# Performance work log

Hardware: AMD Instinct MI355X
Metric: run time of the kernel (lower is better)

Reference implementation:

```python
import jax, jax.numpy as jnp
import numpy as np

N_NODES = 10000
N_EDGES = 640000
N_GRAPHS = 64
D = 128
N_BLOCKS = 2
NEG_SLOPE = 0.01  # F.leaky_relu default


def setup_inputs() -> dict:
    key = jax.random.key(0)
    ks = jax.random.split(key, 9)
    x = jax.random.normal(ks[0], (N_NODES, D), dtype=jnp.float32)
    edge_src = jax.random.randint(ks[1], (N_EDGES,), 0, N_NODES, dtype=jnp.int32)
    edge_dst = jax.random.randint(ks[2], (N_EDGES,), 0, N_NODES, dtype=jnp.int32)
    graph_ids = jnp.sort(jax.random.randint(ks[3], (N_NODES,), 0, N_GRAPHS, dtype=jnp.int32))
    s = 1.414 / np.sqrt(D)  # xavier-normal-ish scale
    Wfc = jax.random.normal(ks[4], (N_BLOCKS, D, D), dtype=jnp.float32) * s
    bfc = jnp.zeros((N_BLOCKS, D), dtype=jnp.float32)
    wl = jax.random.normal(ks[5], (N_BLOCKS, D), dtype=jnp.float32) * s
    wr = jax.random.normal(ks[6], (N_BLOCKS, D), dtype=jnp.float32) * s
    Wres = jax.random.normal(ks[7], (N_BLOCKS, D, D), dtype=jnp.float32) * s
    return {"x": x, "edge_src": edge_src, "edge_dst": edge_dst, "graph_ids": graph_ids,
            "Wfc": Wfc, "bfc": bfc, "wl": wl, "wr": wr, "Wres": Wres}


def _gat_block(x, edge_src, edge_dst, Wfc_b, bfc_b, wl_b, wr_b, Wres_b):
    # node projections: nn.Linear -> x @ W^T + b
    feat = x @ Wfc_b.T + bfc_b                       # [N, D]
    a_self = feat @ wl_b                              # [N] self_a (dst side)
    a_nb = feat @ wr_b                                # [N] attn  (src side)
    # per-edge score: leaky_relu(self_a[dst] + attn[src])
    s = a_self[edge_dst] + a_nb[edge_src]             # [E]
    s = jnp.where(s >= 0, s, NEG_SLOPE * s)
    # segment softmax over incoming edges of each dst node
    m = jax.ops.segment_max(s, edge_dst, num_segments=N_NODES)   # [N]
    e = jnp.exp(s - m[edge_dst])                                  # [E]
    denom = jax.ops.segment_sum(e, edge_dst, num_segments=N_NODES)
    w = e / denom[edge_dst]                                       # [E]
    # attention-weighted neighbor aggregation
    accum = jax.ops.segment_sum(w[:, None] * feat[edge_src], edge_dst,
                                num_segments=N_NODES)             # [N, D]
    # residual (in_size == out_size -> res_fc, no bias), then relu
    out = accum + x @ Wres_b.T
    return jax.nn.relu(out)


def reference(x, edge_src, edge_dst, graph_ids, Wfc, bfc, wl, wr, Wres):
    blocks = [
        _gat_block(x, edge_src, edge_dst, Wfc[b], bfc[b], wl[b], wr[b], Wres[b])
        for b in range(N_BLOCKS)
    ]
    h = jnp.concatenate(blocks, axis=1)               # mode='concat' -> [N, 2*D]
    # dgl.sum_nodes: per-graph sum pooling
    phis = jax.ops.segment_sum(h, graph_ids, num_segments=N_GRAPHS)  # [G, 2*D]
    return h, phis
```

## Files before the change

kernel.cpp:

```cpp
#include <hip/hip_runtime.h>
#include <hip/hip_bf16.h>
#include <math.h>

#define N_NODES 10000
#define N_EDGES 640000
#define N_GRAPHS 64
#define DIM 128
#define NEG_SLOPE 0.01f
#define NB_CSR 128
#define EDGES_PER_BLK (N_EDGES / NB_CSR)

typedef __attribute__((ext_vector_type(8))) short bf16x8;
typedef __attribute__((ext_vector_type(4))) float f32x4;


__device__ __forceinline__ unsigned short f2bf(float f) {
    __hip_bfloat16 h = __float2bfloat16(f);
    return *reinterpret_cast<unsigned short*>(&h);
}

__global__ __launch_bounds__(1024) void csr_hist(const int4* __restrict__ edst4,
                                                 int* __restrict__ bh) {
    __shared__ int hist[N_NODES];
    const int blk = blockIdx.x;
    const int t = threadIdx.x;
    for (int n = t; n < N_NODES; n += 1024) hist[n] = 0;
    __syncthreads();
    const int base4 = blk * (EDGES_PER_BLK / 4);
    for (int i = t; i < EDGES_PER_BLK / 4; i += 1024) {
        int4 d = edst4[base4 + i];
        atomicAdd(&hist[d.x], 1);
        atomicAdd(&hist[d.y], 1);
        atomicAdd(&hist[d.z], 1);
        atomicAdd(&hist[d.w], 1);
    }
    __syncthreads();
    int* dst = bh + (size_t)blk * N_NODES;
    for (int n = t; n < N_NODES; n += 1024) dst[n] = hist[n];
}

__global__ __launch_bounds__(256) void csr_node_scan(int* __restrict__ bh,
                                                     int* __restrict__ deg) {
    int n4 = blockIdx.x * 256 + threadIdx.x;
    if (n4 >= N_NODES / 4) return;
    int4 run = {0, 0, 0, 0};
    for (int blk = 0; blk < NB_CSR; ++blk) {
        int4* p = reinterpret_cast<int4*>(bh + (size_t)blk * N_NODES) + n4;
        int4 v = *p;
        *p = run;
        run.x += v.x; run.y += v.y; run.z += v.z; run.w += v.w;
    }
    reinterpret_cast<int4*>(deg)[n4] = run;
}

__global__ __launch_bounds__(1024) void scan_deg(const int* __restrict__ deg,
                                                 int* __restrict__ rowptr,
                                                 float* __restrict__ phis) {
    __shared__ int sdata[1024];
    const int tid = threadIdx.x;
    for (int i = tid; i < N_GRAPHS * 2 * DIM; i += 1024) phis[i] = 0.f;

    const int base = tid * 10;
    int cnt = N_NODES - base;
    if (cnt < 0) cnt = 0;
    if (cnt > 10) cnt = 10;
    int local[10];
    int s = 0;
    for (int i = 0; i < cnt; ++i) { local[i] = s; s += deg[base + i]; }
    sdata[tid] = s;
    __syncthreads();
    for (int off = 1; off < 1024; off <<= 1) {
        int v = 0;
        if (tid >= off) v = sdata[tid - off];
        __syncthreads();
        if (tid >= off) sdata[tid] += v;
        __syncthreads();
    }
    int pre = (tid == 0) ? 0 : sdata[tid - 1];
    for (int i = 0; i < cnt; ++i) rowptr[base + i] = pre + local[i];
    if (tid == 1023) rowptr[N_NODES] = sdata[1023];
}

__global__ __launch_bounds__(1024) void csr_scatter(
    const int4* __restrict__ esrc4, const int4* __restrict__ edst4,
    const int* __restrict__ rowptr, const int* __restrict__ bh,
    int* __restrict__ csr_src) {
    __shared__ int cur[N_NODES];
    const int blk = blockIdx.x;
    const int t = threadIdx.x;
    const int* boff = bh + (size_t)blk * N_NODES;
    for (int n = t; n < N_NODES; n += 1024) cur[n] = rowptr[n] + boff[n];
    __syncthreads();
    const int base4 = blk * (EDGES_PER_BLK / 4);
    for (int i = t; i < EDGES_PER_BLK / 4; i += 1024) {
        int4 s = esrc4[base4 + i];
        int4 d = edst4[base4 + i];
        csr_src[atomicAdd(&cur[d.x], 1)] = s.x;
        csr_src[atomicAdd(&cur[d.y], 1)] = s.y;
        csr_src[atomicAdd(&cur[d.z], 1)] = s.z;
        csr_src[atomicAdd(&cur[d.w], 1)] = s.w;
    }
}

__global__ __launch_bounds__(256) void gemm_mfma(
    const float* __restrict__ x, const float* __restrict__ Wfc,
    const float* __restrict__ bfc, const float* __restrict__ Wres,
    const float* __restrict__ wl, const float* __restrict__ wr,
    float* __restrict__ resid, unsigned short* __restrict__ feat_b16,
    float* __restrict__ a_self, float* __restrict__ a_nb) {
    const int which = blockIdx.y & 1;
    const int b = blockIdx.y >> 1;
    const float* __restrict__ W = (which ? Wres : Wfc) + b * DIM * DIM;
    const int n0 = blockIdx.x * 64;
    const int t = threadIdx.x;

    __shared__ unsigned short xs[64][136];
    __shared__ unsigned short wsh[128][136];

    {
        const int r = t >> 2, qq = t & 3;
        const int n = n0 + r;
        ushort4* drow = reinterpret_cast<ushort4*>(&xs[r][qq * 32]);
        if (n < N_NODES) {
            const float4* p = reinterpret_cast<const float4*>(x + (size_t)n * DIM + qq * 32);
#pragma unroll
            for (int i = 0; i < 8; ++i) {
                float4 v = p[i];
                ushort4 u;
                u.x = f2bf(v.x); u.y = f2bf(v.y); u.z = f2bf(v.z); u.w = f2bf(v.w);
                drow[i] = u;
            }
        } else {
            ushort4 z = {0, 0, 0, 0};
#pragma unroll
            for (int i = 0; i < 8; ++i) drow[i] = z;
        }
    }
    {
        const int rw = t >> 1, hh = t & 1;
        const float4* p = reinterpret_cast<const float4*>(W + (size_t)rw * DIM + hh * 64);
        ushort4* drow = reinterpret_cast<ushort4*>(&wsh[rw][hh * 64]);
#pragma unroll
        for (int i = 0; i < 16; ++i) {
            float4 v = p[i];
            ushort4 u;
            u.x = f2bf(v.x); u.y = f2bf(v.y); u.z = f2bf(v.z); u.w = f2bf(v.w);
            drow[i] = u;
        }
    }
    __syncthreads();

    const int wave = t >> 6, lane = t & 63;
    const int quad = lane >> 4, jc = lane & 15;
    const int m0 = wave * 16;

    bf16x8 af[4];
#pragma unroll
    for (int ks = 0; ks < 4; ++ks)
        af[ks] = *reinterpret_cast<const bf16x8*>(&xs[m0 + jc][ks * 32 + quad * 8]);

    f32x4 accs[8];
    float ps[4] = {0.f, 0.f, 0.f, 0.f}, pr[4] = {0.f, 0.f, 0.f, 0.f};
#pragma unroll
    for (int jt = 0; jt < 8; ++jt) {
        f32x4 acc = {0.f, 0.f, 0.f, 0.f};
#pragma unroll
        for (int ks = 0; ks < 4; ++ks) {
            bf16x8 bfr = *reinterpret_cast<const bf16x8*>(
                &wsh[jt * 16 + jc][ks * 32 + quad * 8]);
            acc = __builtin_amdgcn_mfma_f32_16x16x32_bf16(af[ks], bfr, acc, 0, 0, 0);
        }
        if (!which) {
            float bias = bfc[b * DIM + jt * 16 + jc];
            acc[0] += bias; acc[1] += bias; acc[2] += bias; acc[3] += bias;
            float wlv = wl[b * DIM + jt * 16 + jc];
            float wrv = wr[b * DIM + jt * 16 + jc];
#pragma unroll
            for (int r2 = 0; r2 < 4; ++r2) { ps[r2] += acc[r2] * wlv; pr[r2] += acc[r2] * wrv; }
        }
        accs[jt] = acc;
    }

    __syncthreads();

    if (!which) {
#pragma unroll
        for (int off = 8; off > 0; off >>= 1) {
#pragma unroll
            for (int r2 = 0; r2 < 4; ++r2) {
                ps[r2] += __shfl_xor(ps[r2], off, 64);
                pr[r2] += __shfl_xor(pr[r2], off, 64);
            }
        }
        if (jc == 0) {
#pragma unroll
            for (int r2 = 0; r2 < 4; ++r2) {
                int n = n0 + m0 + quad * 4 + r2;
                if (n < N_NODES) {
                    a_self[b * N_NODES + n] = ps[r2];
                    a_nb[b * N_NODES + n] = pr[r2];
                }
            }
        }
#pragma unroll
        for (int jt = 0; jt < 8; ++jt)
#pragma unroll
            for (int r2 = 0; r2 < 4; ++r2)
                xs[m0 + quad * 4 + r2][jt * 16 + jc] = f2bf(accs[jt][r2]);
        __syncthreads();
        const int r = t >> 2, qq = t & 3;
        const int n = n0 + r;
        if (n < N_NODES) {
            uint4* dst = reinterpret_cast<uint4*>(
                feat_b16 + ((size_t)b * N_NODES + n) * DIM + qq * 32);
            const uint4* srcp = reinterpret_cast<const uint4*>(&xs[r][qq * 32]);
#pragma unroll
            for (int i = 0; i < 4; ++i) dst[i] = srcp[i];
        }
    } else {
        float* fs = reinterpret_cast<float*>(wsh);
#pragma unroll
        for (int jt = 0; jt < 8; ++jt)
#pragma unroll
            for (int r2 = 0; r2 < 4; ++r2)
                fs[(m0 + quad * 4 + r2) * 136 + jt * 16 + jc] = accs[jt][r2];
        __syncthreads();
        const int r = t >> 2, qq = t & 3;
        const int n = n0 + r;
        if (n < N_NODES) {
            float4* dst = reinterpret_cast<float4*>(
                resid + ((size_t)b * N_NODES + n) * DIM + qq * 32);
            const float4* srcp = reinterpret_cast<const float4*>(&fs[r * 136 + qq * 32]);
#pragma unroll
            for (int i = 0; i < 8; ++i) dst[i] = srcp[i];
        }
    }
}

__global__ __launch_bounds__(256) void aggregate(
    const unsigned short* __restrict__ feat_b16, const float* __restrict__ resid,
    const float* __restrict__ a_self, const float* __restrict__ a_nb,
    const int* __restrict__ rowptr, const int* __restrict__ csr_src,
    float* __restrict__ out) {
    const int wave = threadIdx.x >> 6;
    const int lane = threadIdx.x & 63;
    const int n = blockIdx.x * 4 + wave;
    const int b = blockIdx.y;
    const int q = lane >> 4;
    const int l16 = lane & 15;
    const int start = rowptr[n];
    const int end = rowptr[n + 1];

    const float* __restrict__ anb = a_nb + b * N_NODES;
    const uint4* __restrict__ fb =
        reinterpret_cast<const uint4*>(feat_b16 + (size_t)b * N_NODES * DIM);
    const float asl = a_self[b * N_NODES + n];

    float acc[8];
#pragma unroll
    for (int k = 0; k < 8; ++k) acc[k] = 0.f;
    float dpart = 0.f;

    for (int c = start; c < end; c += 64) {
        int j = c + lane;
        float e = 0.f;
        int src = 0;
        if (j < end) {
            src = csr_src[j];
            float s = asl + anb[src];
            s = (s >= 0.f) ? s : NEG_SLOPE * s;
            e = __expf(s);
        }
        dpart += e;
        int cnt = end - c;
        if (cnt > 64) cnt = 64;
        int iters = (cnt + 3) >> 2;

        float w0 = __shfl(e, q, 64);
        int s0 = __shfl(src, q, 64);
        uint4 f0 = fb[(size_t)s0 * 16 + l16];

        for (int i2 = 0; i2 < iters - 1; ++i2) {
            int idx = (i2 + 1) * 4 + q;
            float w1 = __shfl(e, idx, 64);
            int s1 = __shfl(src, idx, 64);
            uint4 f1 = fb[(size_t)s1 * 16 + l16];
#pragma unroll
            for (int k = 0; k < 4; ++k) {
                unsigned int u = (&f0.x)[k];
                float lo = __uint_as_float(u << 16);
                float hi = __uint_as_float(u & 0xffff0000u);
                acc[2 * k]     += w0 * lo;
                acc[2 * k + 1] += w0 * hi;
            }
            w0 = w1; f0 = f1;
        }
#pragma unroll
        for (int k = 0; k < 4; ++k) {
            unsigned int u = (&f0.x)[k];
            float lo = __uint_as_float(u << 16);
            float hi = __uint_as_float(u & 0xffff0000u);
            acc[2 * k]     += w0 * lo;
            acc[2 * k + 1] += w0 * hi;
        }
    }

#pragma unroll
    for (int k = 0; k < 8; ++k) {
        acc[k] += __shfl_xor(acc[k], 16, 64);
        acc[k] += __shfl_xor(acc[k], 32, 64);
    }
    float denom = dpart;
#pragma unroll
    for (int off = 32; off > 0; off >>= 1) denom += __shfl_xor(denom, off, 64);

    if (q == 0) {
        float inv = (end > start) ? 1.f / denom : 0.f;
        const float4* rr = reinterpret_cast<const float4*>(
            resid + ((size_t)b * N_NODES + n) * DIM);
        float4 r0 = rr[l16 * 2];
        float4 r1 = rr[l16 * 2 + 1];
        float4 o0, o1;
        o0.x = fmaxf(acc[0] * inv + r0.x, 0.f);
        o0.y = fmaxf(acc[1] * inv + r0.y, 0.f);
        o0.z = fmaxf(acc[2] * inv + r0.z, 0.f);
        o0.w = fmaxf(acc[3] * inv + r0.w, 0.f);
        o1.x = fmaxf(acc[4] * inv + r1.x, 0.f);
        o1.y = fmaxf(acc[5] * inv + r1.y, 0.f);
        o1.z = fmaxf(acc[6] * inv + r1.z, 0.f);
        o1.w = fmaxf(acc[7] * inv + r1.w, 0.f);
        float4* po = reinterpret_cast<float4*>(out + (size_t)n * (2 * DIM) + b * DIM);
        po[l16 * 2] = o0;
        po[l16 * 2 + 1] = o1;
    }
}

__device__ int lower_bound_dev(const int* __restrict__ a, int n, int key) {
    int lo = 0, hi = n;
    while (lo < hi) {
        int mid = (lo + hi) >> 1;
        if (a[mid] < key) lo = mid + 1;
        else hi = mid;
    }
    return lo;
}

__global__ __launch_bounds__(256) void pool_graphs(
    const float* __restrict__ h, const int* __restrict__ gids,
    float* __restrict__ phis) {
    const int g = blockIdx.x;
    const int chunk = blockIdx.y;
    const int tid = threadIdx.x;
    int lo = lower_bound_dev(gids, N_NODES, g);
    int hi = lower_bound_dev(gids, N_NODES, g + 1);
    float acc = 0.f;
    for (int n = lo + chunk; n < hi; n += 16) acc += h[(size_t)n * (2 * DIM) + tid];
    if (acc != 0.f) atomicAdd(&phis[(size_t)g * (2 * DIM) + tid], acc);
}

extern "C" void kernel_launch(void* const* d_in, const int* in_sizes, int n_in,
                              void* d_out, int out_size, void* d_ws, size_t ws_size,
                              hipStream_t stream) {
    const float* x    = (const float*)d_in[0];
    const int* esrc   = (const int*)d_in[1];
    const int* edst   = (const int*)d_in[2];
    const int* gids   = (const int*)d_in[3];
    const float* Wfc  = (const float*)d_in[4];
    const float* bfc  = (const float*)d_in[5];
    const float* wl   = (const float*)d_in[6];
    const float* wr   = (const float*)d_in[7];
    const float* Wres = (const float*)d_in[8];
    float* out = (float*)d_out;

    char* ws = (char*)d_ws;
    float* resid   = (float*)(ws + 0);
    float* a_self  = (float*)(ws + 10240000);
    float* a_nb    = (float*)(ws + 10320000);
    int*   deg     = (int*)(ws + 10400000);
    int*   rowptr  = (int*)(ws + 10440000);
    int*   csr_src = (int*)(ws + 10480032);
    unsigned short* feat_b16 = (unsigned short*)(ws + 13040032);
    int*   bh      = (int*)(ws + 18160032);

    float* phis = out + (size_t)N_NODES * 2 * DIM;

    csr_hist<<<NB_CSR, 1024, 0, stream>>>((const int4*)edst, bh);
    csr_node_scan<<<(N_NODES / 4 + 255) / 256, 256, 0, stream>>>(bh, deg);
    scan_deg<<<1, 1024, 0, stream>>>(deg, rowptr, phis);
    csr_scatter<<<NB_CSR, 1024, 0, stream>>>(
        (const int4*)esrc, (const int4*)edst, rowptr, bh, csr_src);

    gemm_mfma<<<dim3((N_NODES + 63) / 64, 4), 256, 0, stream>>>(
        x, Wfc, bfc, Wres, wl, wr, resid, feat_b16, a_self, a_nb);
    aggregate<<<dim3(2500, 2), 256, 0, stream>>>(
        feat_b16, resid, a_self, a_nb, rowptr, csr_src, out);
    pool_graphs<<<dim3(N_GRAPHS, 16), 256, 0, stream>>>(out, gids, phis);
}
```

Measured before the change: 169.8 us.

## Fuse histogram with projection GEMM and split each node's edges across two waves

The CSR histogram blocks and the MFMA projection GEMM blocks now run in one launch, with blocks picking their role by index, so the independent GEMM overlaps the histogram and one kernel launch is removed. The histogram blocks drop from 1024 to 256 threads to match the GEMM's block size. Aggregation now gives each destination node two waves that take alternating 64-edge chunks. Their partial sums and denominators are combined through shared memory before the epilogue. This doubles parallelism for the memory-bound gather, at the cost of an extra block sync and shared-memory reduction.

```diff
diff --git a/kernel.cpp b/kernel.cpp
--- a/kernel.cpp
+++ b/kernel.cpp
@@ -9,6 +9,8 @@
 #define NEG_SLOPE 0.01f
 #define NB_CSR 128
 #define EDGES_PER_BLK (N_EDGES / NB_CSR)
+#define G_TILES 157
+#define G_BLOCKS (G_TILES * 4)
 
 typedef __attribute__((ext_vector_type(8))) short bf16x8;
 typedef __attribute__((ext_vector_type(4))) float f32x4;
@@ -19,24 +21,164 @@
     return *reinterpret_cast<unsigned short*>(&h);
 }
 
-__global__ __launch_bounds__(1024) void csr_hist(const int4* __restrict__ edst4,
-                                                 int* __restrict__ bh) {
-    __shared__ int hist[N_NODES];
-    const int blk = blockIdx.x;
+__global__ __launch_bounds__(256) void gemm_hist(
+    const int4* __restrict__ edst4, int* __restrict__ bh,
+    const float* __restrict__ x, const float* __restrict__ Wfc,
+    const float* __restrict__ bfc, const float* __restrict__ Wres,
+    const float* __restrict__ wl, const float* __restrict__ wr,
+    float* __restrict__ resid, unsigned short* __restrict__ feat_b16,
+    float* __restrict__ a_self, float* __restrict__ a_nb) {
+    __shared__ char smem[52224];
     const int t = threadIdx.x;
-    for (int n = t; n < N_NODES; n += 1024) hist[n] = 0;
+
+    if (blockIdx.x < NB_CSR) {
+        int* hist = reinterpret_cast<int*>(smem);
+        const int blk = blockIdx.x;
+        for (int n = t; n < N_NODES; n += 256) hist[n] = 0;
+        __syncthreads();
+        const int base4 = blk * (EDGES_PER_BLK / 4);
+        for (int i = t; i < EDGES_PER_BLK / 4; i += 256) {
+            int4 d = edst4[base4 + i];
+            atomicAdd(&hist[d.x], 1);
+            atomicAdd(&hist[d.y], 1);
+            atomicAdd(&hist[d.z], 1);
+            atomicAdd(&hist[d.w], 1);
+        }
+        __syncthreads();
+        int* dst = bh + (size_t)blk * N_NODES;
+        for (int n = t; n < N_NODES; n += 256) dst[n] = hist[n];
+        return;
+    }
+
+    const int blk = blockIdx.x - NB_CSR;
+    const int which = blk & 1;
+    const int b = (blk >> 1) & 1;
+    const int n0 = (blk >> 2) * 64;
+    const float* __restrict__ W = (which ? Wres : Wfc) + b * DIM * DIM;
+
+    typedef unsigned short us_row[136];
+    us_row* xs = reinterpret_cast<us_row*>(smem);
+    us_row* wsh = reinterpret_cast<us_row*>(smem + 17408);
+
+    {
+        const int r = t >> 2, qq = t & 3;
+        const int n = n0 + r;
+        ushort4* drow = reinterpret_cast<ushort4*>(&xs[r][qq * 32]);
+        if (n < N_NODES) {
+            const float4* p = reinterpret_cast<const float4*>(x + (size_t)n * DIM + qq * 32);
+#pragma unroll
+            for (int i = 0; i < 8; ++i) {
+                float4 v = p[i];
+                ushort4 u;
+                u.x = f2bf(v.x); u.y = f2bf(v.y); u.z = f2bf(v.z); u.w = f2bf(v.w);
+                drow[i] = u;
+            }
+        } else {
+            ushort4 z = {0, 0, 0, 0};
+#pragma unroll
+            for (int i = 0; i < 8; ++i) drow[i] = z;
+        }
+    }
+    {
+        const int rw = t >> 1, hh = t & 1;
+        const float4* p = reinterpret_cast<const float4*>(W + (size_t)rw * DIM + hh * 64);
+        ushort4* drow = reinterpret_cast<ushort4*>(&wsh[rw][hh * 64]);
+#pragma unroll
+        for (int i = 0; i < 16; ++i) {
+            float4 v = p[i];
+            ushort4 u;
+            u.x = f2bf(v.x); u.y = f2bf(v.y); u.z = f2bf(v.z); u.w = f2bf(v.w);
+            drow[i] = u;
+        }
+    }
     __syncthreads();
-    const int base4 = blk * (EDGES_PER_BLK / 4);
-    for (int i = t; i < EDGES_PER_BLK / 4; i += 1024) {
-        int4 d = edst4[base4 + i];
-        atomicAdd(&hist[d.x], 1);
-        atomicAdd(&hist[d.y], 1);
-        atomicAdd(&hist[d.z], 1);
-        atomicAdd(&hist[d.w], 1);
-    }
+
+    const int wave = t >> 6, lane = t & 63;
+    const int quad = lane >> 4, jc = lane & 15;
+    const int m0 = wave * 16;
+
+    bf16x8 af[4];
+#pragma unroll
+    for (int ks = 0; ks < 4; ++ks)
+        af[ks] = *reinterpret_cast<const bf16x8*>(&xs[m0 + jc][ks * 32 + quad * 8]);
+
+    f32x4 accs[8];
+    float ps[4] = {0.f, 0.f, 0.f, 0.f}, pr[4] = {0.f, 0.f, 0.f, 0.f};
+#pragma unroll
+    for (int jt = 0; jt < 8; ++jt) {
+        f32x4 acc = {0.f, 0.f, 0.f, 0.f};
+#pragma unroll
+        for (int ks = 0; ks < 4; ++ks) {
+            bf16x8 bfr = *reinterpret_cast<const bf16x8*>(
+                &wsh[jt * 16 + jc][ks * 32 + quad * 8]);
+            acc = __builtin_amdgcn_mfma_f32_16x16x32_bf16(af[ks], bfr, acc, 0, 0, 0);
+        }
+        if (!which) {
+            float bias = bfc[b * DIM + jt * 16 + jc];
+            acc[0] += bias; acc[1] += bias; acc[2] += bias; acc[3] += bias;
+            float wlv = wl[b * DIM + jt * 16 + jc];
+            float wrv = wr[b * DIM + jt * 16 + jc];
+#pragma unroll
+            for (int r2 = 0; r2 < 4; ++r2) { ps[r2] += acc[r2] * wlv; pr[r2] += acc[r2] * wrv; }
+        }
+        accs[jt] = acc;
+    }
+
     __syncthreads();
-    int* dst = bh + (size_t)blk * N_NODES;
-    for (int n = t; n < N_NODES; n += 1024) dst[n] = hist[n];
+
+    if (!which) {
+#pragma unroll
+        for (int off = 8; off > 0; off >>= 1) {
+#pragma unroll
+            for (int r2 = 0; r2 < 4; ++r2) {
+                ps[r2] += __shfl_xor(ps[r2], off, 64);
+                pr[r2] += __shfl_xor(pr[r2], off, 64);
+            }
+        }
+        if (jc == 0) {
+#pragma unroll
+            for (int r2 = 0; r2 < 4; ++r2) {
+                int n = n0 + m0 + quad * 4 + r2;
+                if (n < N_NODES) {
+                    a_self[b * N_NODES + n] = ps[r2];
+                    a_nb[b * N_NODES + n] = pr[r2];
+                }
+            }
+        }
+#pragma unroll
+        for (int jt = 0; jt < 8; ++jt)
+#pragma unroll
+            for (int r2 = 0; r2 < 4; ++r2)
+                xs[m0 + quad * 4 + r2][jt * 16 + jc] = f2bf(accs[jt][r2]);
+        __syncthreads();
+        const int r = t >> 2, qq = t & 3;
+        const int n = n0 + r;
+        if (n < N_NODES) {
+            uint4* dst = reinterpret_cast<uint4*>(
+                feat_b16 + ((size_t)b * N_NODES + n) * DIM + qq * 32);
+            const uint4* srcp = reinterpret_cast<const uint4*>(&xs[r][qq * 32]);
+#pragma unroll
+            for (int i = 0; i < 4; ++i) dst[i] = srcp[i];
+        }
+    } else {
+        float* fs = reinterpret_cast<float*>(smem);
+        __syncthreads();
+#pragma unroll
+        for (int jt = 0; jt < 8; ++jt)
+#pragma unroll
+            for (int r2 = 0; r2 < 4; ++r2)
+                fs[(m0 + quad * 4 + r2) * 136 + jt * 16 + jc] = accs[jt][r2];
+        __syncthreads();
+        const int r = t >> 2, qq = t & 3;
+        const int n = n0 + r;
+        if (n < N_NODES) {
+            float4* dst = reinterpret_cast<float4*>(
+                resid + ((size_t)b * N_NODES + n) * DIM + qq * 32);
+            const float4* srcp = reinterpret_cast<const float4*>(&fs[r * 136 + qq * 32]);
+#pragma unroll
+            for (int i = 0; i < 8; ++i) dst[i] = srcp[i];
+        }
+    }
 }
 
 __global__ __launch_bounds__(256) void csr_node_scan(int* __restrict__ bh,
@@ -102,155 +244,25 @@
     }
 }
 
-__global__ __launch_bounds__(256) void gemm_mfma(
-    const float* __restrict__ x, const float* __restrict__ Wfc,
-    const float* __restrict__ bfc, const float* __restrict__ Wres,
-    const float* __restrict__ wl, const float* __restrict__ wr,
-    float* __restrict__ resid, unsigned short* __restrict__ feat_b16,
-    float* __restrict__ a_self, float* __restrict__ a_nb) {
-    const int which = blockIdx.y & 1;
-    const int b = blockIdx.y >> 1;
-    const float* __restrict__ W = (which ? Wres : Wfc) + b * DIM * DIM;
-    const int n0 = blockIdx.x * 64;
-    const int t = threadIdx.x;
-
-    __shared__ unsigned short xs[64][136];
-    __shared__ unsigned short wsh[128][136];
-
-    {
-        const int r = t >> 2, qq = t & 3;
-        const int n = n0 + r;
-        ushort4* drow = reinterpret_cast<ushort4*>(&xs[r][qq * 32]);
-        if (n < N_NODES) {
-            const float4* p = reinterpret_cast<const float4*>(x + (size_t)n * DIM + qq * 32);
-#pragma unroll
-            for (int i = 0; i < 8; ++i) {
-                float4 v = p[i];
-                ushort4 u;
-                u.x = f2bf(v.x); u.y = f2bf(v.y); u.z = f2bf(v.z); u.w = f2bf(v.w);
-                drow[i] = u;
-            }
-        } else {
-            ushort4 z = {0, 0, 0, 0};
-#pragma unroll
-            for (int i = 0; i < 8; ++i) drow[i] = z;
-        }
-    }
-    {
-        const int rw = t >> 1, hh = t & 1;
-        const float4* p = reinterpret_cast<const float4*>(W + (size_t)rw * DIM + hh * 64);
-        ushort4* drow = reinterpret_cast<ushort4*>(&wsh[rw][hh * 64]);
-#pragma unroll
-        for (int i = 0; i < 16; ++i) {
-            float4 v = p[i];
-            ushort4 u;
-            u.x = f2bf(v.x); u.y = f2bf(v.y); u.z = f2bf(v.z); u.w = f2bf(v.w);
-            drow[i] = u;
-        }
-    }
-    __syncthreads();
-
-    const int wave = t >> 6, lane = t & 63;
-    const int quad = lane >> 4, jc = lane & 15;
-    const int m0 = wave * 16;
-
-    bf16x8 af[4];
-#pragma unroll
-    for (int ks = 0; ks < 4; ++ks)
-        af[ks] = *reinterpret_cast<const bf16x8*>(&xs[m0 + jc][ks * 32 + quad * 8]);
-
-    f32x4 accs[8];
-    float ps[4] = {0.f, 0.f, 0.f, 0.f}, pr[4] = {0.f, 0.f, 0.f, 0.f};
-#pragma unroll
-    for (int jt = 0; jt < 8; ++jt) {
-        f32x4 acc = {0.f, 0.f, 0.f, 0.f};
-#pragma unroll
-        for (int ks = 0; ks < 4; ++ks) {
-            bf16x8 bfr = *reinterpret_cast<const bf16x8*>(
-                &wsh[jt * 16 + jc][ks * 32 + quad * 8]);
-            acc = __builtin_amdgcn_mfma_f32_16x16x32_bf16(af[ks], bfr, acc, 0, 0, 0);
-        }
-        if (!which) {
-            float bias = bfc[b * DIM + jt * 16 + jc];
-            acc[0] += bias; acc[1] += bias; acc[2] += bias; acc[3] += bias;
-            float wlv = wl[b * DIM + jt * 16 + jc];
-            float wrv = wr[b * DIM + jt * 16 + jc];
-#pragma unroll
-            for (int r2 = 0; r2 < 4; ++r2) { ps[r2] += acc[r2] * wlv; pr[r2] += acc[r2] * wrv; }
-        }
-        accs[jt] = acc;
-    }
-
-    __syncthreads();
-
-    if (!which) {
-#pragma unroll
-        for (int off = 8; off > 0; off >>= 1) {
-#pragma unroll
-            for (int r2 = 0; r2 < 4; ++r2) {
-                ps[r2] += __shfl_xor(ps[r2], off, 64);
-                pr[r2] += __shfl_xor(pr[r2], off, 64);
-            }
-        }
-        if (jc == 0) {
-#pragma unroll
-            for (int r2 = 0; r2 < 4; ++r2) {
-                int n = n0 + m0 + quad * 4 + r2;
-                if (n < N_NODES) {
-                    a_self[b * N_NODES + n] = ps[r2];
-                    a_nb[b * N_NODES + n] = pr[r2];
-                }
-            }
-        }
-#pragma unroll
-        for (int jt = 0; jt < 8; ++jt)
-#pragma unroll
-            for (int r2 = 0; r2 < 4; ++r2)
-                xs[m0 + quad * 4 + r2][jt * 16 + jc] = f2bf(accs[jt][r2]);
-        __syncthreads();
-        const int r = t >> 2, qq = t & 3;
-        const int n = n0 + r;
-        if (n < N_NODES) {
-            uint4* dst = reinterpret_cast<uint4*>(
-                feat_b16 + ((size_t)b * N_NODES + n) * DIM + qq * 32);
-            const uint4* srcp = reinterpret_cast<const uint4*>(&xs[r][qq * 32]);
-#pragma unroll
-            for (int i = 0; i < 4; ++i) dst[i] = srcp[i];
-        }
-    } else {
-        float* fs = reinterpret_cast<float*>(wsh);
-#pragma unroll
-        for (int jt = 0; jt < 8; ++jt)
-#pragma unroll
-            for (int r2 = 0; r2 < 4; ++r2)
-                fs[(m0 + quad * 4 + r2) * 136 + jt * 16 + jc] = accs[jt][r2];
-        __syncthreads();
-        const int r = t >> 2, qq = t & 3;
-        const int n = n0 + r;
-        if (n < N_NODES) {
-            float4* dst = reinterpret_cast<float4*>(
-                resid + ((size_t)b * N_NODES + n) * DIM + qq * 32);
-            const float4* srcp = reinterpret_cast<const float4*>(&fs[r * 136 + qq * 32]);
-#pragma unroll
-            for (int i = 0; i < 8; ++i) dst[i] = srcp[i];
-        }
-    }
-}
-
 __global__ __launch_bounds__(256) void aggregate(
     const unsigned short* __restrict__ feat_b16, const float* __restrict__ resid,
     const float* __restrict__ a_self, const float* __restrict__ a_nb,
     const int* __restrict__ rowptr, const int* __restrict__ csr_src,
     float* __restrict__ out) {
-    const int wave = threadIdx.x >> 6;
-    const int lane = threadIdx.x & 63;
-    const int n = blockIdx.x * 4 + wave;
+    const int t = threadIdx.x;
+    const int wave = t >> 6, lane = t & 63;
+    const int nl = wave >> 1;
+    const int sub = wave & 1;
+    const int n = blockIdx.x * 2 + nl;
     const int b = blockIdx.y;
     const int q = lane >> 4;
     const int l16 = lane & 15;
     const int start = rowptr[n];
     const int end = rowptr[n + 1];
 
+    __shared__ float pacc[2][2][128];
+    __shared__ float pden[2][2];
+
     const float* __restrict__ anb = a_nb + b * N_NODES;
     const uint4* __restrict__ fb =
         reinterpret_cast<const uint4*>(feat_b16 + (size_t)b * N_NODES * DIM);
@@ -261,7 +273,7 @@
     for (int k = 0; k < 8; ++k) acc[k] = 0.f;
     float dpart = 0.f;
 
-    for (int c = start; c < end; c += 64) {
+    for (int c = start + sub * 64; c < end; c += 128) {
         int j = c + lane;
         float e = 0.f;
         int src = 0;
@@ -310,28 +322,29 @@
         acc[k] += __shfl_xor(acc[k], 16, 64);
         acc[k] += __shfl_xor(acc[k], 32, 64);
     }
-    float denom = dpart;
-#pragma unroll
-    for (int off = 32; off > 0; off >>= 1) denom += __shfl_xor(denom, off, 64);
+    float den = dpart;
+#pragma unroll
+    for (int off = 32; off > 0; off >>= 1) den += __shfl_xor(den, off, 64);
 
     if (q == 0) {
+#pragma unroll
+        for (int k = 0; k < 8; ++k) pacc[nl][sub][l16 * 8 + k] = acc[k];
+    }
+    if (lane == 0) pden[nl][sub] = den;
+    __syncthreads();
+
+    if (sub == 0) {
+        float denom = pden[nl][0] + pden[nl][1];
         float inv = (end > start) ? 1.f / denom : 0.f;
-        const float4* rr = reinterpret_cast<const float4*>(
-            resid + ((size_t)b * N_NODES + n) * DIM);
-        float4 r0 = rr[l16 * 2];
-        float4 r1 = rr[l16 * 2 + 1];
-        float4 o0, o1;
-        o0.x = fmaxf(acc[0] * inv + r0.x, 0.f);
-        o0.y = fmaxf(acc[1] * inv + r0.y, 0.f);
-        o0.z = fmaxf(acc[2] * inv + r0.z, 0.f);
-        o0.w = fmaxf(acc[3] * inv + r0.w, 0.f);
-        o1.x = fmaxf(acc[4] * inv + r1.x, 0.f);
-        o1.y = fmaxf(acc[5] * inv + r1.y, 0.f);
-        o1.z = fmaxf(acc[6] * inv + r1.z, 0.f);
-        o1.w = fmaxf(acc[7] * inv + r1.w, 0.f);
-        float4* po = reinterpret_cast<float4*>(out + (size_t)n * (2 * DIM) + b * DIM);
-        po[l16 * 2] = o0;
-        po[l16 * 2 + 1] = o1;
+        int c0 = lane * 2;
+        float a0 = pacc[nl][0][c0] + pacc[nl][1][c0];
+        float a1 = pacc[nl][0][c0 + 1] + pacc[nl][1][c0 + 1];
+        float2 r = reinterpret_cast<const float2*>(
+            resid + ((size_t)b * N_NODES + n) * DIM)[lane];
+        float2 o;
+        o.x = fmaxf(a0 * inv + r.x, 0.f);
+        o.y = fmaxf(a1 * inv + r.y, 0.f);
+        reinterpret_cast<float2*>(out + (size_t)n * (2 * DIM) + b * DIM)[lane] = o;
     }
 }
 
@@ -384,15 +397,15 @@
 
     float* phis = out + (size_t)N_NODES * 2 * DIM;
 
-    csr_hist<<<NB_CSR, 1024, 0, stream>>>((const int4*)edst, bh);
+    gemm_hist<<<NB_CSR + G_BLOCKS, 256, 0, stream>>>(
+        (const int4*)edst, bh, x, Wfc, bfc, Wres, wl, wr,
+        resid, feat_b16, a_self, a_nb);
     csr_node_scan<<<(N_NODES / 4 + 255) / 256, 256, 0, stream>>>(bh, deg);
     scan_deg<<<1, 1024, 0, stream>>>(deg, rowptr, phis);
     csr_scatter<<<NB_CSR, 1024, 0, stream>>>(
         (const int4*)esrc, (const int4*)edst, rowptr, bh, csr_src);
 
-    gemm_mfma<<<dim3((N_NODES + 63) / 64, 4), 256, 0, stream>>>(
-        x, Wfc, bfc, Wres, wl, wr, resid, feat_b16, a_self, a_nb);
-    aggregate<<<dim3(2500, 2), 256, 0, stream>>>(
+    aggregate<<<dim3(5000, 2), 256, 0, stream>>>(
         feat_b16, resid, a_self, a_nb, rowptr, csr_src, out);
     pool_graphs<<<dim3(N_GRAPHS, 16), 256, 0, stream>>>(out, gids, phis);
 }
```

Result: no change. 172.4 us (+1.6%).

## Fuse edge score computation into CSR scatter, shrink residual and histogram to 16-bit

Applied to the files above, without the earlier changes.

Moves the GEMM ahead of CSR construction so csr_scatter can compute the leaky-relu exp score per edge for both blocks and store (src, exp) pairs. The aggregate kernel then reads precomputed weights instead of gathering a_nb per edge. The residual is stored as bf16 instead of fp32, and per-block histograms as 16-bit, which roughly halves those buffers' traffic. The costs are more scatter work and random reads inside csr_scatter, twice the CSR storage, and lower residual precision. Skipping the max subtraction in the softmax risks overflow.

```diff
diff --git a/kernel.cpp b/kernel.cpp
--- a/kernel.cpp
+++ b/kernel.cpp
@@ -19,8 +19,130 @@
     return *reinterpret_cast<unsigned short*>(&h);
 }
 
+__global__ __launch_bounds__(256) void gemm_mfma(
+    const float* __restrict__ x, const float* __restrict__ Wfc,
+    const float* __restrict__ bfc, const float* __restrict__ Wres,
+    const float* __restrict__ wl, const float* __restrict__ wr,
+    unsigned short* __restrict__ resid_b16, unsigned short* __restrict__ feat_b16,
+    float* __restrict__ a_self, float* __restrict__ a_nb) {
+    const int which = blockIdx.y & 1;
+    const int b = blockIdx.y >> 1;
+    const float* __restrict__ W = (which ? Wres : Wfc) + b * DIM * DIM;
+    const int n0 = blockIdx.x * 64;
+    const int t = threadIdx.x;
+
+    __shared__ unsigned short xs[64][136];
+    __shared__ unsigned short wsh[128][136];
+
+    {
+        const int r = t >> 2, qq = t & 3;
+        const int n = n0 + r;
+        ushort4* drow = reinterpret_cast<ushort4*>(&xs[r][qq * 32]);
+        if (n < N_NODES) {
+            const float4* p = reinterpret_cast<const float4*>(x + (size_t)n * DIM + qq * 32);
+#pragma unroll
+            for (int i = 0; i < 8; ++i) {
+                float4 v = p[i];
+                ushort4 u;
+                u.x = f2bf(v.x); u.y = f2bf(v.y); u.z = f2bf(v.z); u.w = f2bf(v.w);
+                drow[i] = u;
+            }
+        } else {
+            ushort4 z = {0, 0, 0, 0};
+#pragma unroll
+            for (int i = 0; i < 8; ++i) drow[i] = z;
+        }
+    }
+    {
+        const int rw = t >> 1, hh = t & 1;
+        const float4* p = reinterpret_cast<const float4*>(W + (size_t)rw * DIM + hh * 64);
+        ushort4* drow = reinterpret_cast<ushort4*>(&wsh[rw][hh * 64]);
+#pragma unroll
+        for (int i = 0; i < 16; ++i) {
+            float4 v = p[i];
+            ushort4 u;
+            u.x = f2bf(v.x); u.y = f2bf(v.y); u.z = f2bf(v.z); u.w = f2bf(v.w);
+            drow[i] = u;
+        }
+    }
+    __syncthreads();
+
+    const int wave = t >> 6, lane = t & 63;
+    const int quad = lane >> 4, jc = lane & 15;
+    const int m0 = wave * 16;
+
+    bf16x8 af[4];
+#pragma unroll
+    for (int ks = 0; ks < 4; ++ks)
+        af[ks] = *reinterpret_cast<const bf16x8*>(&xs[m0 + jc][ks * 32 + quad * 8]);
+
+    f32x4 accs[8];
+    float ps[4] = {0.f, 0.f, 0.f, 0.f}, pr[4] = {0.f, 0.f, 0.f, 0.f};
+#pragma unroll
+    for (int jt = 0; jt < 8; ++jt) {
+        f32x4 acc = {0.f, 0.f, 0.f, 0.f};
+#pragma unroll
+        for (int ks = 0; ks < 4; ++ks) {
+            bf16x8 bfr = *reinterpret_cast<const bf16x8*>(
+                &wsh[jt * 16 + jc][ks * 32 + quad * 8]);
+            acc = __builtin_amdgcn_mfma_f32_16x16x32_bf16(af[ks], bfr, acc, 0, 0, 0);
+        }
+        if (!which) {
+            float bias = bfc[b * DIM + jt * 16 + jc];
+            acc[0] += bias; acc[1] += bias; acc[2] += bias; acc[3] += bias;
+            float wlv = wl[b * DIM + jt * 16 + jc];
+            float wrv = wr[b * DIM + jt * 16 + jc];
+#pragma unroll
+            for (int r2 = 0; r2 < 4; ++r2) { ps[r2] += acc[r2] * wlv; pr[r2] += acc[r2] * wrv; }
+        }
+        accs[jt] = acc;
+    }
+
+    __syncthreads();
+
+    if (!which) {
+#pragma unroll
+        for (int off = 8; off > 0; off >>= 1) {
+#pragma unroll
+            for (int r2 = 0; r2 < 4; ++r2) {
+                ps[r2] += __shfl_xor(ps[r2], off, 64);
+                pr[r2] += __shfl_xor(pr[r2], off, 64);
+            }
+        }
+        if (jc == 0) {
+#pragma unroll
+            for (int r2 = 0; r2 < 4; ++r2) {
+                int n = n0 + m0 + quad * 4 + r2;
+                if (n < N_NODES) {
+                    a_self[b * N_NODES + n] = ps[r2];
+                    a_nb[b * N_NODES + n] = pr[r2];
+                }
+            }
+        }
+    }
+
+    unsigned short* dst_buf = which ? resid_b16 : feat_b16;
+#pragma unroll
+    for (int jt = 0; jt < 8; ++jt)
+#pragma unroll
+        for (int r2 = 0; r2 < 4; ++r2)
+            xs[m0 + quad * 4 + r2][jt * 16 + jc] = f2bf(accs[jt][r2]);
+    __syncthreads();
+    {
+        const int r = t >> 2, qq = t & 3;
+        const int n = n0 + r;
+        if (n < N_NODES) {
+            uint4* dst = reinterpret_cast<uint4*>(
+                dst_buf + ((size_t)b * N_NODES + n) * DIM + qq * 32);
+            const uint4* srcp = reinterpret_cast<const uint4*>(&xs[r][qq * 32]);
+#pragma unroll
+            for (int i = 0; i < 4; ++i) dst[i] = srcp[i];
+        }
+    }
+}
+
 __global__ __launch_bounds__(1024) void csr_hist(const int4* __restrict__ edst4,
-                                                 int* __restrict__ bh) {
+                                                 unsigned short* __restrict__ bh16) {
     __shared__ int hist[N_NODES];
     const int blk = blockIdx.x;
     const int t = threadIdx.x;
@@ -35,22 +157,34 @@
         atomicAdd(&hist[d.w], 1);
     }
     __syncthreads();
-    int* dst = bh + (size_t)blk * N_NODES;
-    for (int n = t; n < N_NODES; n += 1024) dst[n] = hist[n];
-}
-
-__global__ __launch_bounds__(256) void csr_node_scan(int* __restrict__ bh,
+    unsigned short* dst = bh16 + (size_t)blk * N_NODES;
+    for (int n = t; n < N_NODES; n += 1024) dst[n] = (unsigned short)hist[n];
+}
+
+__device__ __forceinline__ unsigned int pack16(int a, int b) {
+    return (a & 0xffff) | (b << 16);
+}
+
+__global__ __launch_bounds__(256) void csr_node_scan(unsigned short* __restrict__ bh16,
                                                      int* __restrict__ deg) {
-    int n4 = blockIdx.x * 256 + threadIdx.x;
-    if (n4 >= N_NODES / 4) return;
-    int4 run = {0, 0, 0, 0};
+    int n8 = blockIdx.x * 256 + threadIdx.x;
+    if (n8 >= N_NODES / 8) return;
+    int run[8] = {0, 0, 0, 0, 0, 0, 0, 0};
     for (int blk = 0; blk < NB_CSR; ++blk) {
-        int4* p = reinterpret_cast<int4*>(bh + (size_t)blk * N_NODES) + n4;
-        int4 v = *p;
-        *p = run;
-        run.x += v.x; run.y += v.y; run.z += v.z; run.w += v.w;
-    }
-    reinterpret_cast<int4*>(deg)[n4] = run;
+        uint4* p = reinterpret_cast<uint4*>(bh16 + (size_t)blk * N_NODES) + n8;
+        uint4 v = *p;
+        uint4 o;
+        o.x = pack16(run[0], run[1]); o.y = pack16(run[2], run[3]);
+        o.z = pack16(run[4], run[5]); o.w = pack16(run[6], run[7]);
+        *p = o;
+        run[0] += v.x & 0xffff; run[1] += v.x >> 16;
+        run[2] += v.y & 0xffff; run[3] += v.y >> 16;
+        run[4] += v.z & 0xffff; run[5] += v.z >> 16;
+        run[6] += v.w & 0xffff; run[7] += v.w >> 16;
+    }
+    int4* d4 = reinterpret_cast<int4*>(deg) + n8 * 2;
+    d4[0] = make_int4(run[0], run[1], run[2], run[3]);
+    d4[1] = make_int4(run[4], run[5], run[6], run[7]);
 }
 
 __global__ __launch_bounds__(1024) void scan_deg(const int* __restrict__ deg,
@@ -83,164 +217,44 @@
 
 __global__ __launch_bounds__(1024) void csr_scatter(
     const int4* __restrict__ esrc4, const int4* __restrict__ edst4,
-    const int* __restrict__ rowptr, const int* __restrict__ bh,
-    int* __restrict__ csr_src) {
+    const int* __restrict__ rowptr, const unsigned short* __restrict__ bh16,
+    const float* __restrict__ a_self, const float* __restrict__ a_nb,
+    int2* __restrict__ csr_sw) {
     __shared__ int cur[N_NODES];
     const int blk = blockIdx.x;
     const int t = threadIdx.x;
-    const int* boff = bh + (size_t)blk * N_NODES;
-    for (int n = t; n < N_NODES; n += 1024) cur[n] = rowptr[n] + boff[n];
-    __syncthreads();
+    const unsigned short* boff = bh16 + (size_t)blk * N_NODES;
+    for (int n = t; n < N_NODES; n += 1024) cur[n] = rowptr[n] + (int)boff[n];
+    __syncthreads();
+    const float* __restrict__ asl0 = a_self;
+    const float* __restrict__ asl1 = a_self + N_NODES;
+    const float* __restrict__ anb0 = a_nb;
+    const float* __restrict__ anb1 = a_nb + N_NODES;
+    int2* __restrict__ sw0 = csr_sw;
+    int2* __restrict__ sw1 = csr_sw + N_EDGES;
     const int base4 = blk * (EDGES_PER_BLK / 4);
     for (int i = t; i < EDGES_PER_BLK / 4; i += 1024) {
         int4 s = esrc4[base4 + i];
         int4 d = edst4[base4 + i];
-        csr_src[atomicAdd(&cur[d.x], 1)] = s.x;
-        csr_src[atomicAdd(&cur[d.y], 1)] = s.y;
-        csr_src[atomicAdd(&cur[d.z], 1)] = s.z;
-        csr_src[atomicAdd(&cur[d.w], 1)] = s.w;
-    }
-}
-
-__global__ __launch_bounds__(256) void gemm_mfma(
-    const float* __restrict__ x, const float* __restrict__ Wfc,
-    const float* __restrict__ bfc, const float* __restrict__ Wres,
-    const float* __restrict__ wl, const float* __restrict__ wr,
-    float* __restrict__ resid, unsigned short* __restrict__ feat_b16,
-    float* __restrict__ a_self, float* __restrict__ a_nb) {
-    const int which = blockIdx.y & 1;
-    const int b = blockIdx.y >> 1;
-    const float* __restrict__ W = (which ? Wres : Wfc) + b * DIM * DIM;
-    const int n0 = blockIdx.x * 64;
-    const int t = threadIdx.x;
-
-    __shared__ unsigned short xs[64][136];
-    __shared__ unsigned short wsh[128][136];
-
-    {
-        const int r = t >> 2, qq = t & 3;
-        const int n = n0 + r;
-        ushort4* drow = reinterpret_cast<ushort4*>(&xs[r][qq * 32]);
-        if (n < N_NODES) {
-            const float4* p = reinterpret_cast<const float4*>(x + (size_t)n * DIM + qq * 32);
-#pragma unroll
-            for (int i = 0; i < 8; ++i) {
-                float4 v = p[i];
-                ushort4 u;
-                u.x = f2bf(v.x); u.y = f2bf(v.y); u.z = f2bf(v.z); u.w = f2bf(v.w);
-                drow[i] = u;
-            }
-        } else {
-            ushort4 z = {0, 0, 0, 0};
-#pragma unroll
-            for (int i = 0; i < 8; ++i) drow[i] = z;
-        }
-    }
-    {
-        const int rw = t >> 1, hh = t & 1;
-        const float4* p = reinterpret_cast<const float4*>(W + (size_t)rw * DIM + hh * 64);
-        ushort4* drow = reinterpret_cast<ushort4*>(&wsh[rw][hh * 64]);
-#pragma unroll
-        for (int i = 0; i < 16; ++i) {
-            float4 v = p[i];
-            ushort4 u;
-            u.x = f2bf(v.x); u.y = f2bf(v.y); u.z = f2bf(v.z); u.w = f2bf(v.w);
-            drow[i] = u;
-        }
-    }
-    __syncthreads();
-
-    const int wave = t >> 6, lane = t & 63;
-    const int quad = lane >> 4, jc = lane & 15;
-    const int m0 = wave * 16;
-
-    bf16x8 af[4];
-#pragma unroll
-    for (int ks = 0; ks < 4; ++ks)
-        af[ks] = *reinterpret_cast<const bf16x8*>(&xs[m0 + jc][ks * 32 + quad * 8]);
-
-    f32x4 accs[8];
-    float ps[4] = {0.f, 0.f, 0.f, 0.f}, pr[4] = {0.f, 0.f, 0.f, 0.f};
-#pragma unroll
-    for (int jt = 0; jt < 8; ++jt) {
-        f32x4 acc = {0.f, 0.f, 0.f, 0.f};
-#pragma unroll
-        for (int ks = 0; ks < 4; ++ks) {
-            bf16x8 bfr = *reinterpret_cast<const bf16x8*>(
-                &wsh[jt * 16 + jc][ks * 32 + quad * 8]);
-            acc = __builtin_amdgcn_mfma_f32_16x16x32_bf16(af[ks], bfr, acc, 0, 0, 0);
-        }
-        if (!which) {
-            float bias = bfc[b * DIM + jt * 16 + jc];
-            acc[0] += bias; acc[1] += bias; acc[2] += bias; acc[3] += bias;
-            float wlv = wl[b * DIM + jt * 16 + jc];
-            float wrv = wr[b * DIM + jt * 16 + jc];
-#pragma unroll
-            for (int r2 = 0; r2 < 4; ++r2) { ps[r2] += acc[r2] * wlv; pr[r2] += acc[r2] * wrv; }
-        }
-        accs[jt] = acc;
-    }
-
-    __syncthreads();
-
-    if (!which) {
-#pragma unroll
-        for (int off = 8; off > 0; off >>= 1) {
-#pragma unroll
-            for (int r2 = 0; r2 < 4; ++r2) {
-                ps[r2] += __shfl_xor(ps[r2], off, 64);
-                pr[r2] += __shfl_xor(pr[r2], off, 64);
-            }
-        }
-        if (jc == 0) {
-#pragma unroll
-            for (int r2 = 0; r2 < 4; ++r2) {
-                int n = n0 + m0 + quad * 4 + r2;
-                if (n < N_NODES) {
-                    a_self[b * N_NODES + n] = ps[r2];
-                    a_nb[b * N_NODES + n] = pr[r2];
-                }
-            }
-        }
-#pragma unroll
-        for (int jt = 0; jt < 8; ++jt)
-#pragma unroll
-            for (int r2 = 0; r2 < 4; ++r2)
-                xs[m0 + quad * 4 + r2][jt * 16 + jc] = f2bf(accs[jt][r2]);
-        __syncthreads();
-        const int r = t >> 2, qq = t & 3;
-        const int n = n0 + r;
-        if (n < N_NODES) {
-            uint4* dst = reinterpret_cast<uint4*>(
-                feat_b16 + ((size_t)b * N_NODES + n) * DIM + qq * 32);
-            const uint4* srcp = reinterpret_cast<const uint4*>(&xs[r][qq * 32]);
-#pragma unroll
-            for (int i = 0; i < 4; ++i) dst[i] = srcp[i];
-        }
-    } else {
-        float* fs = reinterpret_cast<float*>(wsh);
-#pragma unroll
-        for (int jt = 0; jt < 8; ++jt)
-#pragma unroll
-            for (int r2 = 0; r2 < 4; ++r2)
-                fs[(m0 + quad * 4 + r2) * 136 + jt * 16 + jc] = accs[jt][r2];
-        __syncthreads();
-        const int r = t >> 2, qq = t & 3;
-        const int n = n0 + r;
-        if (n < N_NODES) {
-            float4* dst = reinterpret_cast<float4*>(
-                resid + ((size_t)b * N_NODES + n) * DIM + qq * 32);
-            const float4* srcp = reinterpret_cast<const float4*>(&fs[r * 136 + qq * 32]);
-#pragma unroll
-            for (int i = 0; i < 8; ++i) dst[i] = srcp[i];
+#pragma unroll
+        for (int k = 0; k < 4; ++k) {
+            int se = (&s.x)[k];
+            int de = (&d.x)[k];
+            int pos = atomicAdd(&cur[de], 1);
+            float t0 = asl0[de] + anb0[se];
+            t0 = (t0 >= 0.f) ? t0 : NEG_SLOPE * t0;
+            float t1 = asl1[de] + anb1[se];
+            t1 = (t1 >= 0.f) ? t1 : NEG_SLOPE * t1;
+            sw0[pos] = make_int2(se, __float_as_int(__expf(t0)));
+            sw1[pos] = make_int2(se, __float_as_int(__expf(t1)));
         }
     }
 }
 
 __global__ __launch_bounds__(256) void aggregate(
-    const unsigned short* __restrict__ feat_b16, const float* __restrict__ resid,
-    const float* __restrict__ a_self, const float* __restrict__ a_nb,
-    const int* __restrict__ rowptr, const int* __restrict__ csr_src,
+    const unsigned short* __restrict__ feat_b16,
+    const unsigned short* __restrict__ resid_b16,
+    const int2* __restrict__ csr_sw, const int* __restrict__ rowptr,
     float* __restrict__ out) {
     const int wave = threadIdx.x >> 6;
     const int lane = threadIdx.x & 63;
@@ -251,10 +265,9 @@
     const int start = rowptr[n];
     const int end = rowptr[n + 1];
 
-    const float* __restrict__ anb = a_nb + b * N_NODES;
+    const int2* __restrict__ swb = csr_sw + (size_t)b * N_EDGES;
     const uint4* __restrict__ fb =
         reinterpret_cast<const uint4*>(feat_b16 + (size_t)b * N_NODES * DIM);
-    const float asl = a_self[b * N_NODES + n];
 
     float acc[8];
 #pragma unroll
@@ -266,10 +279,9 @@
         float e = 0.f;
         int src = 0;
         if (j < end) {
-            src = csr_src[j];
-            float s = asl + anb[src];
-            s = (s >= 0.f) ? s : NEG_SLOPE * s;
-            e = __expf(s);
+            int2 sw = swb[j];
+            src = sw.x;
+            e = __int_as_float(sw.y);
         }
         dpart += e;
         int cnt = end - c;
@@ -316,19 +328,23 @@
 
     if (q == 0) {
         float inv = (end > start) ? 1.f / denom : 0.f;
-        const float4* rr = reinterpret_cast<const float4*>(
-            resid + ((size_t)b * N_NODES + n) * DIM);
-        float4 r0 = rr[l16 * 2];
-        float4 r1 = rr[l16 * 2 + 1];
+        uint4 rb = reinterpret_cast<const uint4*>(
+            resid_b16 + ((size_t)b * N_NODES + n) * DIM)[l16];
         float4 o0, o1;
-        o0.x = fmaxf(acc[0] * inv + r0.x, 0.f);
-        o0.y = fmaxf(acc[1] * inv + r0.y, 0.f);
-        o0.z = fmaxf(acc[2] * inv + r0.z, 0.f);
-        o0.w = fmaxf(acc[3] * inv + r0.w, 0.f);
-        o1.x = fmaxf(acc[4] * inv + r1.x, 0.f);
-        o1.y = fmaxf(acc[5] * inv + r1.y, 0.f);
-        o1.z = fmaxf(acc[6] * inv + r1.z, 0.f);
-        o1.w = fmaxf(acc[7] * inv + r1.w, 0.f);
+        {
+            unsigned int u = rb.x;
+            o0.x = fmaxf(acc[0] * inv + __uint_as_float(u << 16), 0.f);
+            o0.y = fmaxf(acc[1] * inv + __uint_as_float(u & 0xffff0000u), 0.f);
+            u = rb.y;
+            o0.z = fmaxf(acc[2] * inv + __uint_as_float(u << 16), 0.f);
+            o0.w = fmaxf(acc[3] * inv + __uint_as_float(u & 0xffff0000u), 0.f);
+            u = rb.z;
+            o1.x = fmaxf(acc[4] * inv + __uint_as_float(u << 16), 0.f);
+            o1.y = fmaxf(acc[5] * inv + __uint_as_float(u & 0xffff0000u), 0.f);
+            u = rb.w;
+            o1.z = fmaxf(acc[6] * inv + __uint_as_float(u << 16), 0.f);
+            o1.w = fmaxf(acc[7] * inv + __uint_as_float(u & 0xffff0000u), 0.f);
+        }
         float4* po = reinterpret_cast<float4*>(out + (size_t)n * (2 * DIM) + b * DIM);
         po[l16 * 2] = o0;
         po[l16 * 2 + 1] = o1;
@@ -373,26 +389,27 @@
     float* out = (float*)d_out;
 
     char* ws = (char*)d_ws;
-    float* resid   = (float*)(ws + 0);
-    float* a_self  = (float*)(ws + 10240000);
-    float* a_nb    = (float*)(ws + 10320000);
-    int*   deg     = (int*)(ws + 10400000);
-    int*   rowptr  = (int*)(ws + 10440000);
-    int*   csr_src = (int*)(ws + 10480032);
-    unsigned short* feat_b16 = (unsigned short*)(ws + 13040032);
-    int*   bh      = (int*)(ws + 18160032);
+    float* a_self  = (float*)(ws + 0);
+    float* a_nb    = (float*)(ws + 80000);
+    int*   deg     = (int*)(ws + 160000);
+    int*   rowptr  = (int*)(ws + 200000);
+    int2*  csr_sw  = (int2*)(ws + 240032);
+    unsigned short* feat_b16  = (unsigned short*)(ws + 10480032);
+    unsigned short* resid_b16 = (unsigned short*)(ws + 15600032);
+    unsigned short* bh16      = (unsigned short*)(ws + 20720032);
 
     float* phis = out + (size_t)N_NODES * 2 * DIM;
 
-    csr_hist<<<NB_CSR, 1024, 0, stream>>>((const int4*)edst, bh);
-    csr_node_scan<<<(N_NODES / 4 + 255) / 256, 256, 0, stream>>>(bh, deg);
+    gemm_mfma<<<dim3((N_NODES + 63) / 64, 4), 256, 0, stream>>>(
+        x, Wfc, bfc, Wres, wl, wr, resid_b16, feat_b16, a_self, a_nb);
+
+    csr_hist<<<NB_CSR, 1024, 0, stream>>>((const int4*)edst, bh16);
+    csr_node_scan<<<(N_NODES / 8 + 255) / 256, 256, 0, stream>>>(bh16, deg);
     scan_deg<<<1, 1024, 0, stream>>>(deg, rowptr, phis);
     csr_scatter<<<NB_CSR, 1024, 0, stream>>>(
-        (const int4*)esrc, (const int4*)edst, rowptr, bh, csr_src);
-
-    gemm_mfma<<<dim3((N_NODES + 63) / 64, 4), 256, 0, stream>>>(
-        x, Wfc, bfc, Wres, wl, wr, resid, feat_b16, a_self, a_nb);
+        (const int4*)esrc, (const int4*)edst, rowptr, bh16, a_self, a_nb, csr_sw);
+
     aggregate<<<dim3(2500, 2), 256, 0, stream>>>(
-        feat_b16, resid, a_self, a_nb, rowptr, csr_src, out);
+        feat_b16, resid_b16, csr_sw, rowptr, out);
     pool_graphs<<<dim3(N_GRAPHS, 16), 256, 0, stream>>>(out, gids, phis);
 }
```

After: 189.8 us. 1.12x slower.
